# Kernel tuning notes

Hardware: AMD Instinct MI355X
Metric: run time of the kernel (lower is better)

Reference implementation:

```python
import jax, jax.numpy as jnp
import numpy as np

K_NEIGHBORS = 3  # init kwarg k_neighbors


def setup_inputs() -> dict:
    key = jax.random.key(0)
    k1, k2 = jax.random.split(key)
    q = jax.random.normal(k1, (75, 640, 21, 21), dtype=jnp.float32)
    S = jax.random.normal(k2, (5, 640, 21, 21), dtype=jnp.float32)
    return {"q": q, "S": S, "qAV_num": 1, "SAV_num": 1, "shot_num": 1}


def reference(q, S, qAV_num, SAV_num, shot_num):
    B, C = q.shape[0], q.shape[1]
    # [B, HW, C], L2-normalize each local descriptor over channels
    qd = q.reshape(B, C, -1).transpose(0, 2, 1)
    qd = qd / jnp.linalg.norm(qd, axis=2, keepdims=True)

    N = S.shape[0]
    sd = S.reshape(N, C, -1).transpose(0, 2, 1)  # [N, HW, C]
    sd = sd / jnp.linalg.norm(sd, axis=2, keepdims=True)
    HW = sd.shape[1]
    M = SAV_num * shot_num * HW
    # group support images into classes: [ncls, C, M]
    sup = sd.reshape(-1, M, C).transpose(0, 2, 1)
    ncls = sup.shape[0]

    # cosine similarity: [B, ncls, HW, M]
    ip = jnp.einsum('bqc,ncm->bnqm', qd, sup)
    # split AV groups: [B//qAV, qAV, ncls, HW, M]
    ip = ip.reshape(B // qAV_num, qAV_num, ncls, HW, M)
    # top-k along the query-descriptor (HW) axis (torch dim=-2)
    topk = jax.lax.top_k(jnp.swapaxes(ip, -1, -2), K_NEIGHBORS)[0]  # [..., M, k]
    img2class = topk.sum(axis=(-1, -2))  # [B', qAV, ncls]
    # geometric mean over the AV axis (dim=1)
    sim = jnp.exp(jnp.mean(jnp.log(img2class), axis=1))  # [B', ncls]
    return sim
```

## Files before the change

### kernel.cpp

```cpp
#include <hip/hip_runtime.h>
#include <hip/hip_bf16.h>


#define B_IMGS 75
#define N_CLS  5
#define C_DIM  640
#define HW     441
#define HWP    448
#define NKT    20
#define NRB    28
#define CHUNK  512
#define TPAD   66

typedef __attribute__((ext_vector_type(8))) short  short8;
typedef __attribute__((ext_vector_type(4))) float  float4v;

__device__ __forceinline__ void ins3(float& t0, float& t1, float& t2, float v) {
    float m  = fminf(t0, v);
    t0 = fmaxf(t0, v);
    float m2 = fminf(t1, m);
    t1 = fmaxf(t1, m);
    t2 = fmaxf(t2, m2);
}

__device__ __forceinline__ void glds16(const __hip_bfloat16* g, __hip_bfloat16* l) {
    __builtin_amdgcn_global_load_lds(
        (const __attribute__((address_space(1))) unsigned int*)g,
        (__attribute__((address_space(3))) unsigned int*)l, 16, 0, 0);
}

__global__ __launch_bounds__(256)
void norm_kernel(const float* __restrict__ q, const float* __restrict__ S,
                 float* __restrict__ invn) {
    __shared__ float part[4][64];
    int bid = blockIdx.x;
    int img = bid / 7;
    int h0  = bid % 7;
    const float* src = (img < B_IMGS)
        ? q + (size_t)img * C_DIM * HW
        : S + (size_t)(img - B_IMGS) * C_DIM * HW;
    int t  = threadIdx.x;
    int hl = t & 63;
    int p  = t >> 6;
    int hw = h0 * 64 + hl;
    int hwc = (hw < HW) ? hw : (HW - 1);

    float ss = 0.f;
    for (int c0 = p * 160; c0 < (p + 1) * 160; c0 += 16) {
        float v[16];
#pragma unroll
        for (int j = 0; j < 16; ++j) v[j] = src[(size_t)(c0 + j) * HW + hwc];
#pragma unroll
        for (int j = 0; j < 16; ++j) ss += v[j] * v[j];
    }
    part[p][hl] = ss;
    __syncthreads();
    if (t < 64) {
        float tot = part[0][t] + part[1][t] + part[2][t] + part[3][t];
        invn[img * HWP + h0 * 64 + t] = (h0 * 64 + t < HW) ? rsqrtf(tot) : 0.f;
    }
}

__global__ __launch_bounds__(256)
void pack_kernel(const float* __restrict__ q, const float* __restrict__ S,
                 const float* __restrict__ invn,
                 __hip_bfloat16* __restrict__ qn2, __hip_bfloat16* __restrict__ sn2) {
    __shared__ __hip_bfloat16 tile[128][TPAD];
    int bid = blockIdx.x;
    int img = bid / 35;
    int rem = bid % 35;
    int h0  = rem / 5;
    int ktg = rem % 5;
    const float* src; __hip_bfloat16* dst;
    if (img < B_IMGS) {
        src = q + (size_t)img * C_DIM * HW;
        dst = qn2 + (size_t)img * NRB * NKT * CHUNK;
    } else {
        src = S + (size_t)(img - B_IMGS) * C_DIM * HW;
        dst = sn2 + (size_t)(img - B_IMGS) * NRB * NKT * CHUNK;
    }
    int t  = threadIdx.x;
    int hl = t & 63;
    int p  = t >> 6;
    int hw = h0 * 64 + hl;
    int hwc = (hw < HW) ? hw : (HW - 1);
    float iv = invn[img * HWP + h0 * 64 + hl];

    for (int c0 = p * 32; c0 < p * 32 + 32; c0 += 8) {
        float v[8];
#pragma unroll
        for (int j = 0; j < 8; ++j)
            v[j] = src[(size_t)(ktg * 128 + c0 + j) * HW + hwc];
#pragma unroll
        for (int j = 0; j < 8; ++j)
            tile[c0 + j][hl] = __float2bfloat16(v[j] * iv);
    }
    __syncthreads();

    int tl  = t & 63;
    int row = tl & 15;
    int oct = tl >> 4;
    int rb  = h0 * 4 + p;
    for (int ktl = 0; ktl < 4; ++ktl) {
        int kt = ktg * 4 + ktl;
        short8 v;
#pragma unroll
        for (int j = 0; j < 8; ++j) {
            __hip_bfloat16 hv = tile[ktl * 32 + oct * 8 + j][p * 16 + row];
            v[j] = *(short*)&hv;
        }
        *(short8*)(dst + ((size_t)rb * NKT + kt) * CHUNK + tl * 8) = v;
    }
}

#define LOADSET(aS, bS, kt)                                                     \
    {                                                                           \
        _Pragma("unroll")                                                       \
        for (int r = 0; r < 7; ++r)                                             \
            aS[r] = *(const short8*)(pA + ((size_t)(r * 4 + w) * NKT + (kt)) * CHUNK); \
        _Pragma("unroll")                                                       \
        for (int j = 0; j < 4; ++j)                                             \
            bS[j] = *(const short8*)(pB + ((size_t)j * NKT + (kt)) * CHUNK);    \
    }

#define MFMASET(aS, bS)                                                         \
    {                                                                           \
        _Pragma("unroll")                                                       \
        for (int r = 0; r < 7; ++r)                                             \
            _Pragma("unroll")                                                   \
            for (int j = 0; j < 4; ++j)                                         \
                acc[r][j] = __builtin_amdgcn_mfma_f32_16x16x32_bf16(            \
                    aS[r], bS[j], acc[r][j], 0, 0, 0);                          \
    }

__global__ __launch_bounds__(256, 2)
void gemm_top3_kernel(const __hip_bfloat16* __restrict__ qn2,
                      const __hip_bfloat16* __restrict__ sn2,
                      float* __restrict__ out) {
    __shared__ float mrg[4][64][3];

    int id  = blockIdx.x;
    int xcd = id & 7;
    int j8  = id >> 3;
    int b   = (j8 / 35) * 8 + xcd;
    if (b >= B_IMGS) return;
    int inner = j8 % 35;
    int n  = inner / 7;
    int mt = inner % 7;

    int tid  = threadIdx.x;
    int w    = tid >> 6;
    int lane = tid & 63;
    int c16  = lane & 15;
    int quad = lane >> 4;

    const __hip_bfloat16* pA = qn2 + (size_t)b * NRB * NKT * CHUNK + lane * 8;
    const __hip_bfloat16* pB = sn2 + ((size_t)n * NRB + mt * 4) * NKT * CHUNK + lane * 8;

    float4v acc[7][4];
#pragma unroll
    for (int r = 0; r < 7; ++r)
#pragma unroll
        for (int j = 0; j < 4; ++j)
            acc[r][j] = (float4v){0.f, 0.f, 0.f, 0.f};

    short8 a0[7], b0[4], a1[7], b1[4];
    LOADSET(a0, b0, 0)
    for (int kt = 0; kt < NKT; kt += 2) {
        LOADSET(a1, b1, kt + 1)
        MFMASET(a0, b0)
        if (kt + 2 < NKT) LOADSET(a0, b0, kt + 2)
        MFMASET(a1, b1)
    }

    float T0[4], T1[4], T2[4];
#pragma unroll
    for (int j = 0; j < 4; ++j) { T0[j] = -1e30f; T1[j] = -1e30f; T2[j] = -1e30f; }
#pragma unroll
    for (int r = 0; r < 7; ++r)
#pragma unroll
        for (int j = 0; j < 4; ++j)
#pragma unroll
            for (int g = 0; g < 4; ++g) {
                int row = r * 64 + w * 16 + quad * 4 + g;
                float v = (row < HW) ? acc[r][j][g] : -1e30f;
                ins3(T0[j], T1[j], T2[j], v);
            }

#pragma unroll
    for (int j = 0; j < 4; ++j) {
#pragma unroll
        for (int d = 16; d <= 32; d <<= 1) {
            float o0 = __shfl_xor(T0[j], d, 64);
            float o1 = __shfl_xor(T1[j], d, 64);
            float o2 = __shfl_xor(T2[j], d, 64);
            ins3(T0[j], T1[j], T2[j], o0);
            ins3(T0[j], T1[j], T2[j], o1);
            ins3(T0[j], T1[j], T2[j], o2);
        }
    }

    if (quad == 0) {
#pragma unroll
        for (int j = 0; j < 4; ++j) {
            mrg[w][j * 16 + c16][0] = T0[j];
            mrg[w][j * 16 + c16][1] = T1[j];
            mrg[w][j * 16 + c16][2] = T2[j];
        }
    }
    __syncthreads();
    if (tid < 64) {
        int col = tid;
        float t0 = mrg[0][col][0], t1 = mrg[0][col][1], t2 = mrg[0][col][2];
#pragma unroll
        for (int ww = 1; ww < 4; ++ww) {
            ins3(t0, t1, t2, mrg[ww][col][0]);
            ins3(t0, t1, t2, mrg[ww][col][1]);
            ins3(t0, t1, t2, mrg[ww][col][2]);
        }
        float s = (mt * 64 + col < HW) ? (t0 + t1 + t2) : 0.f;
#pragma unroll
        for (int d = 32; d >= 1; d >>= 1) s += __shfl_xor(s, d, 64);
        if (tid == 0) atomicAdd(&out[b * N_CLS + n], s);
    }
}

extern "C" void kernel_launch(void* const* d_in, const int* in_sizes, int n_in,
                              void* d_out, int out_size, void* d_ws, size_t ws_size,
                              hipStream_t stream) {
    const float* q = (const float*)d_in[0];
    const float* S = (const float*)d_in[1];
    float* out = (float*)d_out;

    char* ws = (char*)d_ws;
    size_t off = 0;
    __hip_bfloat16* qn2 = (__hip_bfloat16*)(ws + off);
    off += (size_t)B_IMGS * NRB * NKT * CHUNK * 2;  off = (off + 255) & ~(size_t)255;
    __hip_bfloat16* sn2 = (__hip_bfloat16*)(ws + off);
    off += (size_t)N_CLS * NRB * NKT * CHUNK * 2;   off = (off + 255) & ~(size_t)255;
    float* invn = (float*)(ws + off);

    hipMemsetAsync(d_out, 0, (size_t)out_size * sizeof(float), stream);

    norm_kernel<<<dim3(80 * 7), dim3(256), 0, stream>>>(q, S, invn);
    pack_kernel<<<dim3(80 * 7 * 5), dim3(256), 0, stream>>>(q, S, invn, qn2, sn2);
    gemm_top3_kernel<<<dim3(8 * 350), dim3(256), 0, stream>>>(qn2, sn2, out);
}
```

Measured before the change: 264.2 us.

## Fuse norm and pack kernels into one prep kernel and fold output memset

Merges the norm computation and the bf16 packing into a single kernel. Each block computes inverse norms for its 64 spatial positions into shared memory, then rereads the source and writes packed MFMA chunks directly, with no LDS transpose tile. The output zeroing moves into block 0 of that kernel, which removes the memset and one launch. In exchange the grid shrinks from 2800 to 560 blocks, and the second read of the fp32 input uses a strided access pattern (16-row groups) that may coalesce poorly.

```diff
diff --git a/kernel.cpp b/kernel.cpp
--- a/kernel.cpp
+++ b/kernel.cpp
@@ -10,7 +10,6 @@
 #define NKT    20
 #define NRB    28
 #define CHUNK  512
-#define TPAD   66
 
 typedef __attribute__((ext_vector_type(8))) short  short8;
 typedef __attribute__((ext_vector_type(4))) float  float4v;
@@ -23,54 +22,20 @@
     t2 = fmaxf(t2, m2);
 }
 
-__device__ __forceinline__ void glds16(const __hip_bfloat16* g, __hip_bfloat16* l) {
-    __builtin_amdgcn_global_load_lds(
-        (const __attribute__((address_space(1))) unsigned int*)g,
-        (__attribute__((address_space(3))) unsigned int*)l, 16, 0, 0);
-}
-
 __global__ __launch_bounds__(256)
-void norm_kernel(const float* __restrict__ q, const float* __restrict__ S,
-                 float* __restrict__ invn) {
+void prep_kernel(const float* __restrict__ q, const float* __restrict__ S,
+                 __hip_bfloat16* __restrict__ qn2, __hip_bfloat16* __restrict__ sn2,
+                 float* __restrict__ out) {
     __shared__ float part[4][64];
+    __shared__ float inv[64];
+
     int bid = blockIdx.x;
+    if (bid == 0) {
+        for (int i = threadIdx.x; i < B_IMGS * N_CLS; i += 256) out[i] = 0.f;
+    }
+
     int img = bid / 7;
     int h0  = bid % 7;
-    const float* src = (img < B_IMGS)
-        ? q + (size_t)img * C_DIM * HW
-        : S + (size_t)(img - B_IMGS) * C_DIM * HW;
-    int t  = threadIdx.x;
-    int hl = t & 63;
-    int p  = t >> 6;
-    int hw = h0 * 64 + hl;
-    int hwc = (hw < HW) ? hw : (HW - 1);
-
-    float ss = 0.f;
-    for (int c0 = p * 160; c0 < (p + 1) * 160; c0 += 16) {
-        float v[16];
-#pragma unroll
-        for (int j = 0; j < 16; ++j) v[j] = src[(size_t)(c0 + j) * HW + hwc];
-#pragma unroll
-        for (int j = 0; j < 16; ++j) ss += v[j] * v[j];
-    }
-    part[p][hl] = ss;
-    __syncthreads();
-    if (t < 64) {
-        float tot = part[0][t] + part[1][t] + part[2][t] + part[3][t];
-        invn[img * HWP + h0 * 64 + t] = (h0 * 64 + t < HW) ? rsqrtf(tot) : 0.f;
-    }
-}
-
-__global__ __launch_bounds__(256)
-void pack_kernel(const float* __restrict__ q, const float* __restrict__ S,
-                 const float* __restrict__ invn,
-                 __hip_bfloat16* __restrict__ qn2, __hip_bfloat16* __restrict__ sn2) {
-    __shared__ __hip_bfloat16 tile[128][TPAD];
-    int bid = blockIdx.x;
-    int img = bid / 35;
-    int rem = bid % 35;
-    int h0  = rem / 5;
-    int ktg = rem % 5;
     const float* src; __hip_bfloat16* dst;
     if (img < B_IMGS) {
         src = q + (size_t)img * C_DIM * HW;
@@ -84,32 +49,44 @@
     int p  = t >> 6;
     int hw = h0 * 64 + hl;
     int hwc = (hw < HW) ? hw : (HW - 1);
-    float iv = invn[img * HWP + h0 * 64 + hl];
-
-    for (int c0 = p * 32; c0 < p * 32 + 32; c0 += 8) {
-        float v[8];
-#pragma unroll
-        for (int j = 0; j < 8; ++j)
-            v[j] = src[(size_t)(ktg * 128 + c0 + j) * HW + hwc];
-#pragma unroll
-        for (int j = 0; j < 8; ++j)
-            tile[c0 + j][hl] = __float2bfloat16(v[j] * iv);
-    }
+
+    float ss = 0.f;
+    for (int c0 = p * 160; c0 < (p + 1) * 160; c0 += 16) {
+        float v[16];
+#pragma unroll
+        for (int j = 0; j < 16; ++j) v[j] = src[(size_t)(c0 + j) * HW + hwc];
+#pragma unroll
+        for (int j = 0; j < 16; ++j) ss += v[j] * v[j];
+    }
+    part[p][hl] = ss;
     __syncthreads();
-
-    int tl  = t & 63;
+    if (t < 64) {
+        float tot = part[0][t] + part[1][t] + part[2][t] + part[3][t];
+        inv[t] = (h0 * 64 + t < HW) ? rsqrtf(tot) : 0.f;
+    }
+    __syncthreads();
+
+    int tl  = hl;
     int row = tl & 15;
     int oct = tl >> 4;
     int rb  = h0 * 4 + p;
-    for (int ktl = 0; ktl < 4; ++ktl) {
-        int kt = ktg * 4 + ktl;
-        short8 v;
+    int hw2 = h0 * 64 + p * 16 + row;
+    int hw2c = (hw2 < HW) ? hw2 : (HW - 1);
+    float iv = inv[p * 16 + row];
+    const float* s2 = src + hw2c;
+#pragma unroll 2
+    for (int kt = 0; kt < NKT; ++kt) {
+        float v[8];
+#pragma unroll
+        for (int j = 0; j < 8; ++j)
+            v[j] = s2[(size_t)(kt * 32 + oct * 8 + j) * HW];
+        short8 o;
 #pragma unroll
         for (int j = 0; j < 8; ++j) {
-            __hip_bfloat16 hv = tile[ktl * 32 + oct * 8 + j][p * 16 + row];
-            v[j] = *(short*)&hv;
-        }
-        *(short8*)(dst + ((size_t)rb * NKT + kt) * CHUNK + tl * 8) = v;
+            __hip_bfloat16 h = __float2bfloat16(v[j] * iv);
+            o[j] = *(short*)&h;
+        }
+        *(short8*)(dst + ((size_t)rb * NKT + kt) * CHUNK + tl * 8) = o;
     }
 }
 
@@ -237,12 +214,7 @@
     __hip_bfloat16* qn2 = (__hip_bfloat16*)(ws + off);
     off += (size_t)B_IMGS * NRB * NKT * CHUNK * 2;  off = (off + 255) & ~(size_t)255;
     __hip_bfloat16* sn2 = (__hip_bfloat16*)(ws + off);
-    off += (size_t)N_CLS * NRB * NKT * CHUNK * 2;   off = (off + 255) & ~(size_t)255;
-    float* invn = (float*)(ws + off);
-
-    hipMemsetAsync(d_out, 0, (size_t)out_size * sizeof(float), stream);
-
-    norm_kernel<<<dim3(80 * 7), dim3(256), 0, stream>>>(q, S, invn);
-    pack_kernel<<<dim3(80 * 7 * 5), dim3(256), 0, stream>>>(q, S, invn, qn2, sn2);
+
+    prep_kernel<<<dim3(80 * 7), dim3(256), 0, stream>>>(q, S, qn2, sn2, out);
     gemm_top3_kernel<<<dim3(8 * 350), dim3(256), 0, stream>>>(qn2, sn2, out);
 }
```

Measured after the change: 256.2 us. 3.0% less time.
